# Performance work log

Hardware: AMD Instinct MI355X
Metric: run time of the kernel (lower is better)

## Reference

```python
import jax, jax.numpy as jnp
import numpy as np

B, NV, NC, D, E = 16, 8192, 4096, 128, 49152


def _gru_cell(x, h, w_ih, w_hh, b_ih, b_hh):
    """torch.nn.GRUCell math; gate order r, z, n; weights are (3D, D)."""
    gi = x @ w_ih.T + b_ih
    gh = h @ w_hh.T + b_hh
    ir, iz, inn = jnp.split(gi, 3, axis=-1)
    hr, hz, hn = jnp.split(gh, 3, axis=-1)
    r = jax.nn.sigmoid(ir + hr)
    z = jax.nn.sigmoid(iz + hz)
    n = jnp.tanh(inn + r * hn)
    return (1.0 - z) * n + z * h


def _msg_net(x, w1, b1, w2, b2):
    # Linear -> exact GELU -> Linear (torch nn.GELU default is erf-based)
    return jax.nn.gelu(x @ w1.T + b1, approximate=False) @ w2.T + b2


def _spmm(feats, src_idx, dst_idx, n_out):
    """Binary sparse-matrix @ dense: gather rows at src_idx, segment-sum to dst_idx.
    feats: (B, N_src, D) -> (B, n_out, D). Equivalent to torch.sparse.mm(H, feats[i])."""
    gathered = feats[:, src_idx, :]  # (B, E, D)
    return jax.vmap(lambda g: jax.ops.segment_sum(g, dst_idx, num_segments=n_out))(gathered)


def setup_inputs() -> dict:
    key = jax.random.key(0)
    ks = jax.random.split(key, 20)
    s = 0.05
    inp = {
        "v_feats": jax.random.normal(ks[0], (B, NV, D), jnp.float32),
        "c_feats": jax.random.normal(ks[1], (B, NC, D), jnp.float32),
        "edge_chk": jax.random.randint(ks[2], (E,), 0, NC, jnp.int32),
        "edge_var": jax.random.randint(ks[3], (E,), 0, NV, jnp.int32),
        # msg_net: Linear(D,D) -> GELU -> Linear(D,D)
        "msg_w1": jax.random.normal(ks[4], (D, D), jnp.float32) * s,
        "msg_b1": jnp.zeros((D,), jnp.float32),
        "msg_w2": jax.random.normal(ks[5], (D, D), jnp.float32) * s,
        "msg_b2": jnp.zeros((D,), jnp.float32),
        # var_update GRUCell(D, D)
        "var_w_ih": jax.random.normal(ks[6], (3 * D, D), jnp.float32) * s,
        "var_w_hh": jax.random.normal(ks[7], (3 * D, D), jnp.float32) * s,
        "var_b_ih": jnp.zeros((3 * D,), jnp.float32),
        "var_b_hh": jnp.zeros((3 * D,), jnp.float32),
        # chk_update GRUCell(D, D)
        "chk_w_ih": jax.random.normal(ks[8], (3 * D, D), jnp.float32) * s,
        "chk_w_hh": jax.random.normal(ks[9], (3 * D, D), jnp.float32) * s,
        "chk_b_ih": jnp.zeros((3 * D,), jnp.float32),
        "chk_b_hh": jnp.zeros((3 * D,), jnp.float32),
    }
    return inp


def reference(v_feats, c_feats, edge_chk, edge_var,
              msg_w1, msg_b1, msg_w2, msg_b2,
              var_w_ih, var_w_hh, var_b_ih, var_b_hh,
              chk_w_ih, chk_w_hh, chk_b_ih, chk_b_hh):
    b, nv, d = v_feats.shape
    nc = c_feats.shape[1]
    # variable -> check: H @ v_feats (H is binary, rows=checks, cols=vars)
    v_to_c = _spmm(v_feats, edge_var, edge_chk, nc)        # (B, NC, D)
    v_to_c = _msg_net(v_to_c, msg_w1, msg_b1, msg_w2, msg_b2)
    c_new = _gru_cell(v_to_c.reshape(-1, d), c_feats.reshape(-1, d),
                      chk_w_ih, chk_w_hh, chk_b_ih, chk_b_hh).reshape(b, nc, d)
    # check -> variable: H^T @ c_new
    c_to_v = _spmm(c_new, edge_chk, edge_var, nv)          # (B, NV, D)
    c_to_v = _msg_net(c_to_v, msg_w1, msg_b1, msg_w2, msg_b2)
    v_new = _gru_cell(c_to_v.reshape(-1, d), v_feats.reshape(-1, d),
                      var_w_ih, var_w_hh, var_b_ih, var_b_hh).reshape(b, nv, d)
    return (v_new, c_new)
```

## Files before the change

### kernel.cpp

```cpp
#include <hip/hip_runtime.h>

using u16 = unsigned short;
using u32 = unsigned int;
using u64 = unsigned long long;
typedef short short8 __attribute__((ext_vector_type(8)));
typedef unsigned short ushort8 __attribute__((ext_vector_type(8)));
typedef float f32x4 __attribute__((ext_vector_type(4)));

#define GB  16
#define GNV 8192
#define GNC 4096
#define GD  128
#define GE  49152

#define MFMA __builtin_amdgcn_mfma_f32_16x16x32_bf16


__device__ __forceinline__ u16 f2bf(float f){
    u32 u = __builtin_bit_cast(u32, f);
    u32 r = (u >> 16) & 1u;
    u += 0x7fffu + r;
    return (u16)(u >> 16);
}

__device__ __forceinline__ float bf2f(u16 x){
    return __builtin_bit_cast(float, (u32)x << 16);
}

__device__ __forceinline__ u32 cvtpk(float lo, float hi){
    u32 r;
    asm("v_cvt_pk_bf16_f32 %0, %1, %2" : "=v"(r) : "v"(lo), "v"(hi));
    return r;
}

__device__ __forceinline__ ushort8 pack8(float4 v0, float4 v1){
    union { u32 u[4]; ushort8 v; } q;
    q.u[0] = cvtpk(v0.x, v0.y); q.u[1] = cvtpk(v0.z, v0.w);
    q.u[2] = cvtpk(v1.x, v1.y); q.u[3] = cvtpk(v1.z, v1.w);
    return q.v;
}

__device__ __forceinline__ u64 pack4(float a, float b, float c, float d){
    return (u64)cvtpk(a, b) | ((u64)cvtpk(c, d) << 32);
}

__device__ __forceinline__ float sigmoidf_(float x){
    return __fdividef(1.f, 1.f + __expf(-x));
}

__device__ __forceinline__ float tanhf_fast(float x){
    float xc = fminf(15.f, fmaxf(-15.f, x));
    float t  = __expf(2.f * xc);
    return __fdividef(t - 1.f, t + 1.f);
}

__device__ __forceinline__ size_t fidx(int r, int c){
    return ((size_t)(r >> 4) << 11) + ((c >> 5) << 9)
         + (((r & 15) + (((c & 31) >> 3) << 4)) << 3) + (c & 7);
}

__device__ __forceinline__ char* swzp(const void* base, int row, int bc){
    return (char*)base + row * 256 + (bc ^ ((row & 7) << 4));
}

__device__ __forceinline__ short8 ldfrag(const u16* tile, int row, int lane, int ks){
    int bc = ks * 64 + ((lane >> 4) << 4);
    return *(const short8*)swzp(tile, row, bc);
}


__global__ void k_hist(const int* __restrict__ ec, const int* __restrict__ ev,
                       int* cc, int* cv){
    int e = blockIdx.x * 256 + threadIdx.x;
    if (e < GE){ atomicAdd(&cc[ec[e]], 1); atomicAdd(&cv[ev[e]], 1); }
}

__global__ __launch_bounds__(1024) void k_scan2(const int* __restrict__ cnt_c, int* off_c, int* cur_c,
                                                const int* __restrict__ cnt_v, int* off_v, int* cur_v){
    const int* cnt = blockIdx.x ? cnt_v : cnt_c;
    int* off = blockIdx.x ? off_v : off_c;
    int* cur = blockIdx.x ? cur_v : cur_c;
    const int n = blockIdx.x ? GNV : GNC;
    __shared__ int part[1024];
    int tid = threadIdx.x;
    int chunk = n >> 10;
    int base = tid * chunk;
    int s = 0;
    for (int i = 0; i < chunk; ++i) s += cnt[base + i];
    part[tid] = s;
    __syncthreads();
    #pragma unroll
    for (int ofs = 1; ofs < 1024; ofs <<= 1){
        int v = (tid >= ofs) ? part[tid - ofs] : 0;
        __syncthreads();
        part[tid] += v;
        __syncthreads();
    }
    if (tid == 1023) off[n] = part[1023];
    int run = part[tid] - s;
    for (int i = 0; i < chunk; ++i){
        off[base + i] = run; cur[base + i] = run; run += cnt[base + i];
    }
}

__global__ void k_fill(const int* __restrict__ ec, const int* __restrict__ ev,
                       int* cur_c, int* lst_c, int* cur_v, int* lst_v){
    int e = blockIdx.x * 256 + threadIdx.x;
    if (e < GE){
        int c = ec[e], v = ev[e];
        lst_c[atomicAdd(&cur_c[c], 1)] = v;
        lst_v[atomicAdd(&cur_v[v], 1)] = c;
    }
}

__global__ void k_sort2(const int* __restrict__ off_c, int* lst_c,
                        const int* __restrict__ off_v, int* lst_v){
    int i = blockIdx.x * 256 + threadIdx.x;
    const int* off; int* lst; int idx;
    if (i < GNC){ off = off_c; lst = lst_c; idx = i; }
    else if (i < GNC + GNV){ off = off_v; lst = lst_v; idx = i - GNC; }
    else return;
    int s = off[idx], e = off[idx + 1];
    for (int a = s + 1; a < e; ++a){
        int v = lst[a]; int b = a - 1;
        while (b >= s && lst[b] > v){ lst[b + 1] = lst[b]; --b; }
        lst[b + 1] = v;
    }
}

__global__ void k_cvt6(const float* __restrict__ s0, const float* __restrict__ s1,
                       const float* __restrict__ s2, const float* __restrict__ s3,
                       const float* __restrict__ s4, const float* __restrict__ s5,
                       u16* __restrict__ dst){
    int i = blockIdx.x * 256 + threadIdx.x;
    const float* s; int off;
    if (i < 16384)       { s = s0; off = i; }
    else if (i < 32768)  { s = s1; off = i - 16384; }
    else if (i < 81920)  { s = s2; off = i - 32768; }
    else if (i < 131072) { s = s3; off = i - 81920; }
    else if (i < 180224) { s = s4; off = i - 131072; }
    else                 { s = s5; off = i - 180224; }
    dst[i] = f2bf(s[off]);
}


__global__ __launch_bounds__(256) void k_trg(const float* __restrict__ vfe,
                                             const float* __restrict__ cfe,
                                             u16* __restrict__ vT, u16* __restrict__ vF,
                                             u16* __restrict__ cF){
    const int t = threadIdx.x;
    const int ks = t >> 6, sub = (t >> 4) & 3, row = t & 15;
    const int c = ks * 32 + sub * 8;
    int gg = blockIdx.x;
    const float* src; u16* dstF; int n, b, node0, grp; u16* dstT = nullptr;
    if (gg < 8192){ b = gg >> 9; node0 = (gg & 511) << 4; grp = gg;
                    src = vfe; dstF = vF; n = GNV; dstT = vT; }
    else { int idx = gg - 8192; b = idx >> 8; node0 = (idx & 255) << 4; grp = idx;
           src = cfe; dstF = cF; n = GNC; }
    const float4* s = (const float4*)(src + ((size_t)b * n + node0 + row) * GD + c);
    float4 v0 = s[0], v1 = s[1];
    ushort8 pk = pack8(v0, v1);
    *(ushort8*)(dstF + ((size_t)grp << 11) + t * 8) = pk;
    if (dstT)
        *(ushort8*)(dstT + ((size_t)(node0 + row) << 11) + b * 128 + c) = pk;
}


__global__ __launch_bounds__(256) void k_tr1(const float* __restrict__ src,
                                             u16* __restrict__ dst, int n){
    const int node = blockIdx.x, t = threadIdx.x;
    const int b = t >> 4, d0 = (t & 15) * 8;
    const float4* s = (const float4*)(src + ((size_t)b * n + node) * GD + d0);
    *(ushort8*)(dst + ((size_t)node << 11) + b * 128 + d0) = pack8(s[0], s[1]);
}


__global__ __launch_bounds__(256) void k_spmm(const u16* __restrict__ srcT,
                                              const int* __restrict__ off,
                                              const int* __restrict__ lst,
                                              u16* __restrict__ dstF, int ndst){
    const int node = blockIdx.x, t = threadIdx.x;
    const int b = t >> 4, d0 = (t & 15) * 8;
    float a0[8], a1[8], a2[8], a3[8];
    #pragma unroll
    for (int i = 0; i < 8; ++i){ a0[i] = 0.f; a1[i] = 0.f; a2[i] = 0.f; a3[i] = 0.f; }
    const int s = off[node], e = off[node + 1];
    const u16* base = srcT + t * 8;
    int a = s;
    for (; a + 4 <= e; a += 4){
        ushort8 v0 = *(const ushort8*)(base + ((size_t)lst[a    ] << 11));
        ushort8 v1 = *(const ushort8*)(base + ((size_t)lst[a + 1] << 11));
        ushort8 v2 = *(const ushort8*)(base + ((size_t)lst[a + 2] << 11));
        ushort8 v3 = *(const ushort8*)(base + ((size_t)lst[a + 3] << 11));
        #pragma unroll
        for (int i = 0; i < 8; ++i){
            a0[i] += bf2f(v0[i]); a1[i] += bf2f(v1[i]);
            a2[i] += bf2f(v2[i]); a3[i] += bf2f(v3[i]);
        }
    }
    for (; a < e; ++a){
        ushort8 v = *(const ushort8*)(base + ((size_t)lst[a] << 11));
        #pragma unroll
        for (int i = 0; i < 8; ++i) a0[i] += bf2f(v[i]);
    }
    float acc[8];
    #pragma unroll
    for (int i = 0; i < 8; ++i) acc[i] = (a0[i] + a1[i]) + (a2[i] + a3[i]);
    u64* p = (u64*)(dstF + fidx(b * ndst + node, d0));
    p[0] = pack4(acc[0], acc[1], acc[2], acc[3]);
    p[1] = pack4(acc[4], acc[5], acc[6], acc[7]);
}


__global__ __launch_bounds__(512) void k_msg(u16* __restrict__ X,
                                             const u16* __restrict__ W1, const float* __restrict__ b1,
                                             const u16* __restrict__ W2, const float* __restrict__ b2,
                                             int ngroups){
    __shared__ __align__(16) u16 Gs[2][16 * 128];
    const int tid = threadIdx.x, lane = tid & 63, w = tid >> 6;
    const int l15 = lane & 15, rg = lane >> 4;
    const int j = w * 16 + l15;

    short8 w1f[4], w2f[4];
    #pragma unroll
    for (int ks = 0; ks < 4; ++ks){
        w1f[ks] = *(const short8*)(W1 + (size_t)j * 128 + ks * 32 + rg * 8);
        w2f[ks] = *(const short8*)(W2 + (size_t)j * 128 + ks * 32 + rg * 8);
    }
    const float bb1 = b1[j], bb2 = b2[j];

    const int stride = gridDim.x;
    const int ng = ngroups / stride;

    short8 xA[4], xB[4];
    auto loadx = [&](short8* xf, int g){
        const u16* xb = X + ((size_t)g << 11);
        #pragma unroll
        for (int ks = 0; ks < 4; ++ks) xf[ks] = *(const short8*)(xb + ks * 512 + lane * 8);
    };
    auto g1 = [&](const short8* xf, int buf){
        f32x4 acc = {0, 0, 0, 0};
        #pragma unroll
        for (int ks = 0; ks < 4; ++ks) acc = MFMA(xf[ks], w1f[ks], acc, 0, 0, 0);
        #pragma unroll
        for (int i = 0; i < 4; ++i){
            float v = acc[i] + bb1;
            float g = 0.5f * v * (1.f + erff(v * 0.70710678f));
            *(u16*)swzp(Gs[buf], rg * 4 + i, j * 2) = f2bf(g);
        }
    };
    auto g2 = [&](int buf, int g){
        f32x4 acc = {0, 0, 0, 0};
        #pragma unroll
        for (int ks = 0; ks < 4; ++ks)
            acc = MFMA(ldfrag(Gs[buf], l15, lane, ks), w2f[ks], acc, 0, 0, 0);
        #pragma unroll
        for (int i = 0; i < 4; ++i)
            X[fidx(g * 16 + rg * 4 + i, j)] = f2bf(acc[i] + bb2);
    };

    int g = blockIdx.x;
    loadx(xA, g);
    g1(xA, 0);
    for (int k = 0; k < ng; k += 2){
        loadx(xB, g + stride);
        __syncthreads();
        g2(0, g);
        g1(xB, 1);
        if (k + 2 < ng) loadx(xA, g + 2 * stride);
        __syncthreads();
        g2(1, g + stride);
        if (k + 2 < ng) g1(xA, 0);
        g += 2 * stride;
    }
}


__global__ __launch_bounds__(512) void k_gru(const u16* __restrict__ XF, const u16* __restrict__ HF,
                                             const u16* __restrict__ Wih, const float* __restrict__ bih,
                                             const u16* __restrict__ Whh, const float* __restrict__ bhh,
                                             float* __restrict__ Out, int ngroups){
    const int tid = threadIdx.x, lane = tid & 63, w = tid >> 6;
    const int l15 = lane & 15, rg = lane >> 4;
    const int j = w * 16 + l15;

    short8 wf[6][4];
    #pragma unroll
    for (int g = 0; g < 3; ++g){
        #pragma unroll
        for (int ks = 0; ks < 4; ++ks){
            wf[g][ks]     = *(const short8*)(Wih + (size_t)(g * 128 + j) * 128 + ks * 32 + rg * 8);
            wf[g + 3][ks] = *(const short8*)(Whh + (size_t)(g * 128 + j) * 128 + ks * 32 + rg * 8);
        }
    }
    const float bir = bih[j]       + bhh[j];
    const float biz = bih[128 + j] + bhh[128 + j];
    const float bin = bih[256 + j];
    const float bhn = bhh[256 + j];

    const int h0off = ((j >> 5) << 9) + (((j & 31) >> 3) << 7) + ((rg * 4) << 3) + (j & 7);

    const int stride = gridDim.x;
    const int ng = ngroups / stride;

    short8 xfA[4], hfA[4], xfB[4], hfB[4];
    float h0A[4], h0B[4];

    auto load = [&](short8* xf, short8* hf, float* h0, int g){
        const u16* xb = XF + ((size_t)g << 11);
        const u16* hb = HF + ((size_t)g << 11);
        #pragma unroll
        for (int ks = 0; ks < 4; ++ks){
            xf[ks] = *(const short8*)(xb + ks * 512 + lane * 8);
            hf[ks] = *(const short8*)(hb + ks * 512 + lane * 8);
        }
        #pragma unroll
        for (int i = 0; i < 4; ++i) h0[i] = bf2f(hb[h0off + i * 8]);
    };

    auto comp = [&](const short8* xf, const short8* hf, const float* h0, int g){
        f32x4 ar = {0,0,0,0}, az = {0,0,0,0}, an = {0,0,0,0}, hn = {0,0,0,0};
        #pragma unroll
        for (int ks = 0; ks < 4; ++ks){
            ar = MFMA(xf[ks], wf[0][ks], ar, 0, 0, 0);
            az = MFMA(xf[ks], wf[1][ks], az, 0, 0, 0);
            an = MFMA(xf[ks], wf[2][ks], an, 0, 0, 0);
            ar = MFMA(hf[ks], wf[3][ks], ar, 0, 0, 0);
            az = MFMA(hf[ks], wf[4][ks], az, 0, 0, 0);
            hn = MFMA(hf[ks], wf[5][ks], hn, 0, 0, 0);
        }
        #pragma unroll
        for (int i = 0; i < 4; ++i){
            int r = g * 16 + rg * 4 + i;
            float rr = sigmoidf_(ar[i] + bir);
            float zz = sigmoidf_(az[i] + biz);
            float nn = tanhf_fast(an[i] + bin + rr * (hn[i] + bhn));
            Out[(size_t)r * GD + j] = (1.f - zz) * nn + zz * h0[i];
        }
    };

    int g = blockIdx.x;
    load(xfA, hfA, h0A, g);
    for (int k = 0; k < ng; k += 2){
        load(xfB, hfB, h0B, g + stride);
        comp(xfA, hfA, h0A, g);
        if (k + 2 < ng) load(xfA, hfA, h0A, g + 2 * stride);
        comp(xfB, hfB, h0B, g + stride);
        g += 2 * stride;
    }
}


extern "C" void kernel_launch(void* const* d_in, const int* in_sizes, int n_in,
                              void* d_out, int out_size, void* d_ws, size_t ws_size,
                              hipStream_t stream){
    const float* v_feats  = (const float*)d_in[0];
    const float* c_feats  = (const float*)d_in[1];
    const int*   edge_chk = (const int*)d_in[2];
    const int*   edge_var = (const int*)d_in[3];
    const float* msg_w1   = (const float*)d_in[4];
    const float* msg_b1   = (const float*)d_in[5];
    const float* msg_w2   = (const float*)d_in[6];
    const float* msg_b2   = (const float*)d_in[7];
    const float* var_w_ih = (const float*)d_in[8];
    const float* var_w_hh = (const float*)d_in[9];
    const float* var_b_ih = (const float*)d_in[10];
    const float* var_b_hh = (const float*)d_in[11];
    const float* chk_w_ih = (const float*)d_in[12];
    const float* chk_w_hh = (const float*)d_in[13];
    const float* chk_b_ih = (const float*)d_in[14];
    const float* chk_b_hh = (const float*)d_in[15];

    float* out_v = (float*)d_out;
    float* out_c = out_v + (size_t)GB * GNV * GD;

    char* p = (char*)d_ws;
    auto take = [&](size_t bytes) -> void* {
        void* r = (void*)p; p += (bytes + 255) & ~(size_t)255; return r;
    };
    int* cnt_c = (int*)take(GNC * 4);
    int* cnt_v = (int*)take(GNV * 4);
    int* off_c = (int*)take((GNC + 1) * 4);
    int* off_v = (int*)take((GNV + 1) * 4);
    int* cur_c = (int*)take(GNC * 4);
    int* cur_v = (int*)take(GNV * 4);
    int* lst_c = (int*)take(GE * 4);
    int* lst_v = (int*)take(GE * 4);
    u16* w1b  = (u16*)take((size_t)GD * GD * 2);
    u16* w2b  = (u16*)take((size_t)GD * GD * 2);
    u16* cihb = (u16*)take((size_t)3 * GD * GD * 2);
    u16* chhb = (u16*)take((size_t)3 * GD * GD * 2);
    u16* vihb = (u16*)take((size_t)3 * GD * GD * 2);
    u16* vhhb = (u16*)take((size_t)3 * GD * GD * 2);
    u16* mc = (u16*)take((size_t)GB * GNC * GD * 2);
    u16* mv = (u16*)take((size_t)GB * GNV * GD * 2);
    u16* vT = (u16*)take((size_t)GNV * GB * GD * 2);
    u16* cT = (u16*)take((size_t)GNC * GB * GD * 2);
    u16* vF = (u16*)take((size_t)GB * GNV * GD * 2);
    u16* cF = (u16*)take((size_t)GB * GNC * GD * 2);

    hipMemsetAsync(cnt_c, 0, (GNC + GNV) * 4, stream);
    k_hist<<<(GE + 255) / 256, 256, 0, stream>>>(edge_chk, edge_var, cnt_c, cnt_v);
    k_scan2<<<2, 1024, 0, stream>>>(cnt_c, off_c, cur_c, cnt_v, off_v, cur_v);
    k_fill<<<(GE + 255) / 256, 256, 0, stream>>>(edge_chk, edge_var, cur_c, lst_c, cur_v, lst_v);
    k_sort2<<<(GNC + GNV + 255) / 256, 256, 0, stream>>>(off_c, lst_c, off_v, lst_v);
    k_cvt6<<<896, 256, 0, stream>>>(msg_w1, msg_w2, chk_w_ih, chk_w_hh, var_w_ih, var_w_hh, w1b);
    k_trg<<<8192 + 4096, 256, 0, stream>>>(v_feats, c_feats, vT, vF, cF);

    k_spmm<<<GNC, 256, 0, stream>>>(vT, off_c, lst_c, mc, GNC);
    k_msg<<<512, 512, 0, stream>>>(mc, w1b, msg_b1, w2b, msg_b2, (GB * GNC) / 16);
    k_gru<<<512, 512, 0, stream>>>(mc, cF, cihb, chk_b_ih, chhb, chk_b_hh,
                                   out_c, (GB * GNC) / 16);
    k_tr1<<<GNC, 256, 0, stream>>>(out_c, cT, GNC);
    k_spmm<<<GNV, 256, 0, stream>>>(cT, off_v, lst_v, mv, GNV);
    k_msg<<<512, 512, 0, stream>>>(mv, w1b, msg_b1, w2b, msg_b2, (GB * GNV) / 16);
    k_gru<<<512, 512, 0, stream>>>(mv, vF, vihb, var_b_ih, vhhb, var_b_hh,
                                   out_v, (GB * GNV) / 16);
}
```

Measured before the change: 352.3 us.

## Fuse message MLP and GRU cell into one kernel via shared-memory staging

Merges the k_msg and k_gru kernels into a single k_msgru kernel. The MLP output is staged in LDS (Ms) and read back as the GRU input fragments, so it no longer makes a bf16 round trip through global memory and one launch per half-iteration is removed. In exchange, each thread holds all weight fragments at once (w1, w2, and six GRU matrices), which raises register pressure. It also adds extra __syncthreads per group and serialises the MLP and GRU stages within a block.

New measurement: 374.1 us. +6.2%, slower.

```diff
diff --git a/kernel.cpp b/kernel.cpp
--- a/kernel.cpp
+++ b/kernel.cpp
@@ -212,79 +212,26 @@
 }
 
 
-__global__ __launch_bounds__(512) void k_msg(u16* __restrict__ X,
-                                             const u16* __restrict__ W1, const float* __restrict__ b1,
-                                             const u16* __restrict__ W2, const float* __restrict__ b2,
-                                             int ngroups){
+__global__ __launch_bounds__(512) void k_msgru(
+    const u16* __restrict__ XF, const u16* __restrict__ HF,
+    const u16* __restrict__ W1, const float* __restrict__ b1,
+    const u16* __restrict__ W2, const float* __restrict__ b2,
+    const u16* __restrict__ Wih, const float* __restrict__ bih,
+    const u16* __restrict__ Whh, const float* __restrict__ bhh,
+    float* __restrict__ Out, int ngroups)
+{
     __shared__ __align__(16) u16 Gs[2][16 * 128];
+    __shared__ __align__(16) u16 Ms[2][16 * 128];
     const int tid = threadIdx.x, lane = tid & 63, w = tid >> 6;
     const int l15 = lane & 15, rg = lane >> 4;
     const int j = w * 16 + l15;
 
-    short8 w1f[4], w2f[4];
+    short8 w1f[4], w2f[4], wf[6][4];
     #pragma unroll
     for (int ks = 0; ks < 4; ++ks){
         w1f[ks] = *(const short8*)(W1 + (size_t)j * 128 + ks * 32 + rg * 8);
         w2f[ks] = *(const short8*)(W2 + (size_t)j * 128 + ks * 32 + rg * 8);
     }
-    const float bb1 = b1[j], bb2 = b2[j];
-
-    const int stride = gridDim.x;
-    const int ng = ngroups / stride;
-
-    short8 xA[4], xB[4];
-    auto loadx = [&](short8* xf, int g){
-        const u16* xb = X + ((size_t)g << 11);
-        #pragma unroll
-        for (int ks = 0; ks < 4; ++ks) xf[ks] = *(const short8*)(xb + ks * 512 + lane * 8);
-    };
-    auto g1 = [&](const short8* xf, int buf){
-        f32x4 acc = {0, 0, 0, 0};
-        #pragma unroll
-        for (int ks = 0; ks < 4; ++ks) acc = MFMA(xf[ks], w1f[ks], acc, 0, 0, 0);
-        #pragma unroll
-        for (int i = 0; i < 4; ++i){
-            float v = acc[i] + bb1;
-            float g = 0.5f * v * (1.f + erff(v * 0.70710678f));
-            *(u16*)swzp(Gs[buf], rg * 4 + i, j * 2) = f2bf(g);
-        }
-    };
-    auto g2 = [&](int buf, int g){
-        f32x4 acc = {0, 0, 0, 0};
-        #pragma unroll
-        for (int ks = 0; ks < 4; ++ks)
-            acc = MFMA(ldfrag(Gs[buf], l15, lane, ks), w2f[ks], acc, 0, 0, 0);
-        #pragma unroll
-        for (int i = 0; i < 4; ++i)
-            X[fidx(g * 16 + rg * 4 + i, j)] = f2bf(acc[i] + bb2);
-    };
-
-    int g = blockIdx.x;
-    loadx(xA, g);
-    g1(xA, 0);
-    for (int k = 0; k < ng; k += 2){
-        loadx(xB, g + stride);
-        __syncthreads();
-        g2(0, g);
-        g1(xB, 1);
-        if (k + 2 < ng) loadx(xA, g + 2 * stride);
-        __syncthreads();
-        g2(1, g + stride);
-        if (k + 2 < ng) g1(xA, 0);
-        g += 2 * stride;
-    }
-}
-
-
-__global__ __launch_bounds__(512) void k_gru(const u16* __restrict__ XF, const u16* __restrict__ HF,
-                                             const u16* __restrict__ Wih, const float* __restrict__ bih,
-                                             const u16* __restrict__ Whh, const float* __restrict__ bhh,
-                                             float* __restrict__ Out, int ngroups){
-    const int tid = threadIdx.x, lane = tid & 63, w = tid >> 6;
-    const int l15 = lane & 15, rg = lane >> 4;
-    const int j = w * 16 + l15;
-
-    short8 wf[6][4];
     #pragma unroll
     for (int g = 0; g < 3; ++g){
         #pragma unroll
@@ -293,6 +240,7 @@
             wf[g + 3][ks] = *(const short8*)(Whh + (size_t)(g * 128 + j) * 128 + ks * 32 + rg * 8);
         }
     }
+    const float bb1 = b1[j], bb2 = b2[j];
     const float bir = bih[j]       + bhh[j];
     const float biz = bih[128 + j] + bhh[128 + j];
     const float bin = bih[256 + j];
@@ -303,10 +251,10 @@
     const int stride = gridDim.x;
     const int ng = ngroups / stride;
 
-    short8 xfA[4], hfA[4], xfB[4], hfB[4];
+    short8 xA[4], xB[4], hA[4], hB[4];
     float h0A[4], h0B[4];
 
-    auto load = [&](short8* xf, short8* hf, float* h0, int g){
+    auto loadg = [&](short8* xf, short8* hf, float* h0, int g){
         const u16* xb = XF + ((size_t)g << 11);
         const u16* hb = HF + ((size_t)g << 11);
         #pragma unroll
@@ -318,13 +266,34 @@
         for (int i = 0; i < 4; ++i) h0[i] = bf2f(hb[h0off + i * 8]);
     };
 
-    auto comp = [&](const short8* xf, const short8* hf, const float* h0, int g){
+    auto g1 = [&](const short8* xf, int buf){
+        f32x4 acc = {0, 0, 0, 0};
+        #pragma unroll
+        for (int ks = 0; ks < 4; ++ks) acc = MFMA(xf[ks], w1f[ks], acc, 0, 0, 0);
+        #pragma unroll
+        for (int i = 0; i < 4; ++i){
+            float v = acc[i] + bb1;
+            float ge = 0.5f * v * (1.f + erff(v * 0.70710678f));
+            *(u16*)swzp(Gs[buf], rg * 4 + i, j * 2) = f2bf(ge);
+        }
+    };
+    auto g2 = [&](int buf){
+        f32x4 acc = {0, 0, 0, 0};
+        #pragma unroll
+        for (int ks = 0; ks < 4; ++ks)
+            acc = MFMA(ldfrag(Gs[buf], l15, lane, ks), w2f[ks], acc, 0, 0, 0);
+        #pragma unroll
+        for (int i = 0; i < 4; ++i)
+            *(u16*)swzp(Ms[buf], rg * 4 + i, j * 2) = f2bf(acc[i] + bb2);
+    };
+    auto gru = [&](int buf, const short8* hf, const float* h0, int g){
         f32x4 ar = {0,0,0,0}, az = {0,0,0,0}, an = {0,0,0,0}, hn = {0,0,0,0};
         #pragma unroll
         for (int ks = 0; ks < 4; ++ks){
-            ar = MFMA(xf[ks], wf[0][ks], ar, 0, 0, 0);
-            az = MFMA(xf[ks], wf[1][ks], az, 0, 0, 0);
-            an = MFMA(xf[ks], wf[2][ks], an, 0, 0, 0);
+            short8 x = ldfrag(Ms[buf], l15, lane, ks);
+            ar = MFMA(x, wf[0][ks], ar, 0, 0, 0);
+            az = MFMA(x, wf[1][ks], az, 0, 0, 0);
+            an = MFMA(x, wf[2][ks], an, 0, 0, 0);
             ar = MFMA(hf[ks], wf[3][ks], ar, 0, 0, 0);
             az = MFMA(hf[ks], wf[4][ks], az, 0, 0, 0);
             hn = MFMA(hf[ks], wf[5][ks], hn, 0, 0, 0);
@@ -340,12 +309,22 @@
     };
 
     int g = blockIdx.x;
-    load(xfA, hfA, h0A, g);
+    loadg(xA, hA, h0A, g);
+    g1(xA, 0);
     for (int k = 0; k < ng; k += 2){
-        load(xfB, hfB, h0B, g + stride);
-        comp(xfA, hfA, h0A, g);
-        if (k + 2 < ng) load(xfA, hfA, h0A, g + 2 * stride);
-        comp(xfB, hfB, h0B, g + stride);
+        const int gA = g, gB = g + stride;
+        loadg(xB, hB, h0B, gB);
+        __syncthreads();
+        g2(0);
+        __syncthreads();
+        gru(0, hA, h0A, gA);
+        g1(xB, 1);
+        if (k + 2 < ng) loadg(xA, hA, h0A, gA + 2 * stride);
+        __syncthreads();
+        g2(1);
+        __syncthreads();
+        gru(1, hB, h0B, gB);
+        if (k + 2 < ng) g1(xA, 0);
         g += 2 * stride;
     }
 }
@@ -408,12 +387,12 @@
     k_trg<<<8192 + 4096, 256, 0, stream>>>(v_feats, c_feats, vT, vF, cF);
 
     k_spmm<<<GNC, 256, 0, stream>>>(vT, off_c, lst_c, mc, GNC);
-    k_msg<<<512, 512, 0, stream>>>(mc, w1b, msg_b1, w2b, msg_b2, (GB * GNC) / 16);
-    k_gru<<<512, 512, 0, stream>>>(mc, cF, cihb, chk_b_ih, chhb, chk_b_hh,
-                                   out_c, (GB * GNC) / 16);
+    k_msgru<<<512, 512, 0, stream>>>(mc, cF, w1b, msg_b1, w2b, msg_b2,
+                                     cihb, chk_b_ih, chhb, chk_b_hh,
+                                     out_c, (GB * GNC) / 16);
     k_tr1<<<GNC, 256, 0, stream>>>(out_c, cT, GNC);
     k_spmm<<<GNV, 256, 0, stream>>>(cT, off_v, lst_v, mv, GNV);
-    k_msg<<<512, 512, 0, stream>>>(mv, w1b, msg_b1, w2b, msg_b2, (GB * GNV) / 16);
-    k_gru<<<512, 512, 0, stream>>>(mv, vF, vihb, var_b_ih, vhhb, var_b_hh,
-                                   out_v, (GB * GNV) / 16);
-}
+    k_msgru<<<512, 512, 0, stream>>>(mv, vF, w1b, msg_b1, w2b, msg_b2,
+                                     vihb, var_b_ih, vhhb, var_b_hh,
+                                     out_v, (GB * GNV) / 16);
+}
```
